# Kernel optimization log

Hardware: AMD Instinct MI355X
Metric: run time of the kernel (lower is better)

The kernel has to match this reference:

```python
import jax, jax.numpy as jnp
import numpy as np

NUM_EMB = 4096
EMB_DIM = 256
COMMIT = 0.25


def setup_inputs() -> dict:
    key = jax.random.key(0)
    k1, k2 = jax.random.split(key)
    z = jax.random.normal(k1, (64, 32, 32, EMB_DIM), dtype=jnp.float32)
    # torch init: uniform(-1/K, 1/K)
    codebook = jax.random.uniform(k2, (NUM_EMB, EMB_DIM), dtype=jnp.float32,
                                  minval=-1.0 / NUM_EMB, maxval=1.0 / NUM_EMB)
    return {"z": z, "codebook": codebook}


def reference(z, codebook):
    zf = z.reshape(-1, EMB_DIM)                       # [N, D]
    # ||z||^2 - 2 z.e + ||e||^2  -> [N, K]
    d = (jnp.sum(zf * zf, axis=1, keepdims=True)
         - 2.0 * (zf @ codebook.T)
         + jnp.sum(codebook * codebook, axis=1))
    idx = jnp.argmin(d, axis=1)                       # [N]
    z_q = codebook[idx].reshape(z.shape)              # gather replaces one-hot matmul
    sg = jax.lax.stop_gradient
    loss = jnp.mean((sg(z_q) - z) ** 2) + COMMIT * jnp.mean((z_q - sg(z)) ** 2)
    z_q_ste = z + sg(z_q - z)                         # straight-through
    return z_q_ste, loss
```

## Files before the change

kernel.cpp:

```cpp
#include <hip/hip_runtime.h>
#include <hip/hip_bf16.h>
#include <stdint.h>

#define NUM_EMB 4096
#define EMB_DIM 256
#define NVEC 65536
#define OUT0_SIZE (NVEC * EMB_DIM)
#define MTILE 128
#define NTILE 64
#define DCONST 0.0625f

typedef __bf16 bf16x8 __attribute__((ext_vector_type(8)));
typedef float floatx16 __attribute__((ext_vector_type(16)));

static __device__ __forceinline__ unsigned int f2bf(float f) {
  unsigned int u = __float_as_uint(f);
  return (u + 0x7fffu + ((u >> 16) & 1u)) >> 16;
}

static __device__ __forceinline__ uint4 pack_bf8(float4 a, float4 b) {
  uint4 r;
  r.x = f2bf(a.x) | (f2bf(a.y) << 16);
  r.y = f2bf(a.z) | (f2bf(a.w) << 16);
  r.z = f2bf(b.x) | (f2bf(b.y) << 16);
  r.w = f2bf(b.z) | (f2bf(b.w) << 16);
  return r;
}

__global__ void __launch_bounds__(256) vq_prep(const float* __restrict__ cbf,
                                               unsigned short* __restrict__ cbb,
                                               float* __restrict__ enorm,
                                               float* __restrict__ out) {
  int w = threadIdx.x >> 6;
  int lane = threadIdx.x & 63;
  int row = blockIdx.x * 4 + w;
  float4 v = ((const float4*)(cbf + (size_t)row * EMB_DIM))[lane];
  float ss = v.x * v.x + v.y * v.y + v.z * v.z + v.w * v.w;
  ushort4 b;
  b.x = (unsigned short)f2bf(v.x);
  b.y = (unsigned short)f2bf(v.y);
  b.z = (unsigned short)f2bf(v.z);
  b.w = (unsigned short)f2bf(v.w);
  ((ushort4*)(cbb + (size_t)row * EMB_DIM))[lane] = b;
#pragma unroll
  for (int m = 1; m < 64; m <<= 1) ss += __shfl_xor(ss, m, 64);
  if (lane == 0) enorm[row] = ss + DCONST;
  if (blockIdx.x == 0 && threadIdx.x == 0) out[OUT0_SIZE] = 0.0f;
}

__global__ void __launch_bounds__(256, 2) vq_main(const float* __restrict__ z,
                                                  const float* __restrict__ cbf,
                                                  const unsigned short* __restrict__ cbb,
                                                  const float* __restrict__ enorm,
                                                  float* __restrict__ out) {
  __shared__ __align__(16) unsigned char sstage[2][NTILE * 512];
  __shared__ unsigned int minlds[2][MTILE];
  __shared__ int idx_lds[MTILE];
  __shared__ float wsum[4];
  __shared__ float zwsum[2];

  const int t = threadIdx.x;
  const int w = t >> 6;
  const int lane = t & 63;
  const int h = lane >> 5;
  const int eL = lane & 31;
  const int rg = w & 1;
  const int cg = w >> 1;
  const int blk = blockIdx.x;
  const int row_base = blk * MTILE + rg * 64;

  auto stage_tile = [&](int buf, int c0) {
#pragma unroll
    for (int j = 0; j < 8; ++j) {
      int e = (w << 4) + (j << 1) + h;
      int s = eL ^ (e & 7);
      const unsigned short* src = cbb + ((size_t)(c0 + e) << 8) + (s << 3);
      __builtin_amdgcn_global_load_lds(
          (const __attribute__((address_space(1))) void*)src,
          (__attribute__((address_space(3))) void*)&sstage[buf][(w << 13) + (j << 10)],
          16, 0, 0);
    }
  };

  stage_tile(0, 0);
  float enC = enorm[cg * 32 + eL];

  uint4 afrag[2][16];
  float zn[2] = {0.f, 0.f};
#pragma unroll
  for (int g = 0; g < 2; ++g) {
    const float* rp = z + (size_t)(row_base + g * 32 + eL) * EMB_DIM + h * 8;
#pragma unroll
    for (int ks = 0; ks < 16; ++ks) {
      float4 a0 = *(const float4*)(rp + ks * 16);
      float4 a1 = *(const float4*)(rp + ks * 16 + 4);
      zn[g] += a0.x * a0.x + a0.y * a0.y + a0.z * a0.z + a0.w * a0.w
             + a1.x * a1.x + a1.y * a1.y + a1.z * a1.z + a1.w * a1.w;
      afrag[g][ks] = pack_bf8(a0, a1);
    }
    zn[g] += __shfl_xor(zn[g], 32, 64);
  }
  if (cg == 0) {
    float zs = zn[0] + zn[1];
#pragma unroll
    for (int m = 1; m <= 16; m <<= 1) zs += __shfl_xor(zs, m, 64);
    if (lane == 0) zwsum[rg] = zs;
  }

  unsigned int pmin[32];
#pragma unroll
  for (int s = 0; s < 32; ++s) pmin[s] = 0xFFFFFFFFu;

  __syncthreads();

  const int sx4 = (eL & 7) << 4;
  int cur = 0;
  for (int c0 = 0; c0 < NUM_EMB; c0 += NTILE) {
    int c1 = c0 + NTILE;
    float enN = enC;
    if (c1 < NUM_EMB) {
      stage_tile(cur ^ 1, c1);
      enN = enorm[c1 + cg * 32 + eL];
    }

    floatx16 acc0, acc1;
#pragma unroll
    for (int r = 0; r < 16; ++r) { acc0[r] = 0.f; acc1[r] = 0.f; }
    const unsigned char* bp = &sstage[cur][(cg * 32 + eL) * 512];
#pragma unroll
    for (int ks = 0; ks < 16; ++ks) {
      uint4 bv = *(const uint4*)(bp + ((ks * 32 + h * 16) ^ sx4));
      bf16x8 b = __builtin_bit_cast(bf16x8, bv);
      acc0 = __builtin_amdgcn_mfma_f32_32x32x16_bf16(
          __builtin_bit_cast(bf16x8, afrag[0][ks]), b, acc0, 0, 0, 0);
      acc1 = __builtin_amdgcn_mfma_f32_32x32x16_bf16(
          __builtin_bit_cast(bf16x8, afrag[1][ks]), b, acc1, 0, 0, 0);
    }

    unsigned int colb = (unsigned int)(c0 + cg * 32 + eL);
#pragma unroll
    for (int reg = 0; reg < 16; ++reg) {
      float d0 = fmaf(-2.f, acc0[reg], enC);
      unsigned int p0 = (__float_as_uint(d0) & 0xFFFFF000u) | colb;
      if (p0 < pmin[reg]) pmin[reg] = p0;
      float d1 = fmaf(-2.f, acc1[reg], enC);
      unsigned int p1 = (__float_as_uint(d1) & 0xFFFFF000u) | colb;
      if (p1 < pmin[16 + reg]) pmin[16 + reg] = p1;
    }

    __syncthreads();
    cur ^= 1;
    enC = enN;
  }

#pragma unroll
  for (int s = 0; s < 32; ++s) {
    unsigned int v = pmin[s];
#pragma unroll
    for (int m = 1; m <= 16; m <<= 1) {
      unsigned int o = __shfl_xor(v, m, 64);
      if (o < v) v = o;
    }
    pmin[s] = v;
  }
  if (eL == 0) {
#pragma unroll
    for (int s = 0; s < 32; ++s) {
      int g = s >> 4, reg = s & 15;
      int rowl = rg * 64 + g * 32 + (reg & 3) + 8 * (reg >> 2) + 4 * h;
      minlds[cg][rowl] = pmin[s];
    }
  }
  __syncthreads();

  float rl = 0.f;
  if (t < MTILE) {
    unsigned int m0 = minlds[0][t], m1 = minlds[1][t];
    unsigned int m = m1 < m0 ? m1 : m0;
    idx_lds[t] = (int)(m & 0xFFFu);
    rl = __uint_as_float(m & 0xFFFFF000u) - DCONST;
  }
#pragma unroll
  for (int m = 1; m < 64; m <<= 1) rl += __shfl_xor(rl, m, 64);
  if (lane == 0) wsum[w] = rl;
  __syncthreads();
  if (t == 0) {
    float s = (wsum[0] + wsum[1]) + (wsum[2] + wsum[3]) + zwsum[0] + zwsum[1];
    atomicAdd(out + OUT0_SIZE, s * (1.25f / (float)OUT0_SIZE));
  }

#pragma unroll 4
  for (int j = 0; j < 32; ++j) {
    int id4 = j * 256 + t;
    int r = id4 >> 6, c4 = id4 & 63;
    int k = idx_lds[r];
    float4 ev = ((const float4*)(cbf + (size_t)k * EMB_DIM))[c4];
    ((float4*)(out + (size_t)(blk * MTILE + r) * EMB_DIM))[c4] = ev;
  }
}

extern "C" void kernel_launch(void* const* d_in, const int* in_sizes, int n_in,
                              void* d_out, int out_size, void* d_ws, size_t ws_size,
                              hipStream_t stream) {
  const float* z = (const float*)d_in[0];
  const float* cbf = (const float*)d_in[1];
  unsigned short* cbb = (unsigned short*)d_ws;
  float* enorm = (float*)((char*)d_ws + (size_t)NUM_EMB * EMB_DIM * 2);
  float* out = (float*)d_out;
  vq_prep<<<NUM_EMB / 4, 256, 0, stream>>>(cbf, cbb, enorm, out);
  vq_main<<<NVEC / MTILE, 256, 0, stream>>>(z, cbf, cbb, enorm, out);
}
```

Measured before the change: 261.7 us.

## Software-pipeline argmin epilogue of previous tile under current tile's MFMAs

Unrolls the codebook loop by two with ping-pong accumulator sets, so the distance and argmin update for the previous 64-code tile interleaves with the MFMA chain of the current tile. The goal is to hide the VALU epilogue behind matrix-core latency rather than running it serially after each tile. The cost is an extra 32 accumulator registers per lane, which could raise VGPR/AGPR pressure under launch_bounds(256,2) and cause spills.

```diff
diff --git a/kernel.cpp b/kernel.cpp
--- a/kernel.cpp
+++ b/kernel.cpp
@@ -83,7 +83,7 @@
   };
 
   stage_tile(0, 0);
-  float enC = enorm[cg * 32 + eL];
+  const int laneoff = cg * 32 + eL;
 
   uint4 afrag[2][16];
   float zn[2] = {0.f, 0.f};
@@ -111,46 +111,68 @@
 #pragma unroll
   for (int s = 0; s < 32; ++s) pmin[s] = 0xFFFFFFFFu;
 
+  floatx16 fz;
+#pragma unroll
+  for (int r = 0; r < 16; ++r) fz[r] = 0.f;
+  floatx16 accE0, accE1, accO0, accO1;
+
   __syncthreads();
 
   const int sx4 = (eL & 7) << 4;
-  int cur = 0;
-  for (int c0 = 0; c0 < NUM_EMB; c0 += NTILE) {
-    int c1 = c0 + NTILE;
-    float enN = enC;
-    if (c1 < NUM_EMB) {
-      stage_tile(cur ^ 1, c1);
-      enN = enorm[c1 + cg * 32 + eL];
-    }
-
-    floatx16 acc0, acc1;
-#pragma unroll
-    for (int r = 0; r < 16; ++r) { acc0[r] = 0.f; acc1[r] = 0.f; }
-    const unsigned char* bp = &sstage[cur][(cg * 32 + eL) * 512];
+  const unsigned char* bpE = &sstage[0][(size_t)laneoff * 512];
+  const unsigned char* bpO = &sstage[1][(size_t)laneoff * 512];
+
+  auto half_step = [&](floatx16& a0, floatx16& a1, const floatx16& p0,
+                       const floatx16& p1, const unsigned char* bp,
+                       bool do_epi, unsigned int colbP, float enP) {
 #pragma unroll
     for (int ks = 0; ks < 16; ++ks) {
       uint4 bv = *(const uint4*)(bp + ((ks * 32 + h * 16) ^ sx4));
       bf16x8 b = __builtin_bit_cast(bf16x8, bv);
-      acc0 = __builtin_amdgcn_mfma_f32_32x32x16_bf16(
-          __builtin_bit_cast(bf16x8, afrag[0][ks]), b, acc0, 0, 0, 0);
-      acc1 = __builtin_amdgcn_mfma_f32_32x32x16_bf16(
-          __builtin_bit_cast(bf16x8, afrag[1][ks]), b, acc1, 0, 0, 0);
-    }
-
-    unsigned int colb = (unsigned int)(c0 + cg * 32 + eL);
-#pragma unroll
-    for (int reg = 0; reg < 16; ++reg) {
-      float d0 = fmaf(-2.f, acc0[reg], enC);
-      unsigned int p0 = (__float_as_uint(d0) & 0xFFFFF000u) | colb;
-      if (p0 < pmin[reg]) pmin[reg] = p0;
-      float d1 = fmaf(-2.f, acc1[reg], enC);
-      unsigned int p1 = (__float_as_uint(d1) & 0xFFFFF000u) | colb;
-      if (p1 < pmin[16 + reg]) pmin[16 + reg] = p1;
-    }
-
+      a0 = __builtin_amdgcn_mfma_f32_32x32x16_bf16(
+          __builtin_bit_cast(bf16x8, afrag[0][ks]), b, ks == 0 ? fz : a0, 0, 0, 0);
+      a1 = __builtin_amdgcn_mfma_f32_32x32x16_bf16(
+          __builtin_bit_cast(bf16x8, afrag[1][ks]), b, ks == 0 ? fz : a1, 0, 0, 0);
+      if (do_epi) {
+        float d0 = fmaf(-2.f, p0[ks], enP);
+        unsigned int q0 = (__float_as_uint(d0) & 0xFFFFF000u) | colbP;
+        pmin[ks] = min(pmin[ks], q0);
+        float d1 = fmaf(-2.f, p1[ks], enP);
+        unsigned int q1 = (__float_as_uint(d1) & 0xFFFFF000u) | colbP;
+        pmin[16 + ks] = min(pmin[16 + ks], q1);
+      }
+    }
+  };
+
+  float enE = enorm[laneoff];
+  float enOdd = 0.f;
+  for (int c0 = 0; c0 < NUM_EMB; c0 += 2 * NTILE) {
+    stage_tile(1, c0 + NTILE);
+    float enOn = enorm[c0 + NTILE + laneoff];
+    half_step(accE0, accE1, accO0, accO1, bpE, c0 > 0,
+              (unsigned int)(c0 - NTILE + laneoff), enOdd);
+    enOdd = enOn;
     __syncthreads();
-    cur ^= 1;
-    enC = enN;
+
+    float enEn = enE;
+    if (c0 + 2 * NTILE < NUM_EMB) {
+      stage_tile(0, c0 + 2 * NTILE);
+      enEn = enorm[c0 + 2 * NTILE + laneoff];
+    }
+    half_step(accO0, accO1, accE0, accE1, bpO, true,
+              (unsigned int)(c0 + laneoff), enE);
+    enE = enEn;
+    __syncthreads();
+  }
+#pragma unroll
+  for (int r = 0; r < 16; ++r) {
+    unsigned int colbP = (unsigned int)(NUM_EMB - NTILE + laneoff);
+    float d0 = fmaf(-2.f, accO0[r], enOdd);
+    unsigned int q0 = (__float_as_uint(d0) & 0xFFFFF000u) | colbP;
+    pmin[r] = min(pmin[r], q0);
+    float d1 = fmaf(-2.f, accO1[r], enOdd);
+    unsigned int q1 = (__float_as_uint(d1) & 0xFFFFF000u) | colbP;
+    pmin[16 + r] = min(pmin[16 + r], q1);
   }
 
 #pragma unroll
```

Result: slower. 370.4 us (+41.5%).

## Software-pipeline argmin epilogue into MFMA chains with interleaved scheduling

Applied to the files above, without the earlier changes.

The codebook loop is unrolled by two tiles, and the distance/argmin epilogue of each accumulator is overlapped with the MFMA chain of the other accumulator. Sched-group barriers interleave the MFMA, LDS read and VALU work, so the epilogue VALU cost is meant to hide under matrix-core latency. This raises live register pressure because both accumulators are held across chains, and it adds tricky bookkeeping for the enorm and column values of the previous tile.

```diff
diff --git a/kernel.cpp b/kernel.cpp
--- a/kernel.cpp
+++ b/kernel.cpp
@@ -48,6 +48,30 @@
   if (blockIdx.x == 0 && threadIdx.x == 0) out[OUT0_SIZE] = 0.0f;
 }
 
+#define ZERO16(ACC)                                   \
+  {                                                   \
+    _Pragma("unroll") for (int r_ = 0; r_ < 16; ++r_) \
+        (ACC)[r_] = 0.f;                              \
+  }
+
+#define CHAIN(BP, ACC, AG, PACC, POFF, DOEPI, ENP, COLBP)                     \
+  {                                                                           \
+    _Pragma("unroll") for (int ks_ = 0; ks_ < 16; ++ks_) {                    \
+      uint4 bv_ = *(const uint4*)((BP) + ((ks_ * 32 + h * 16) ^ sx4));        \
+      bf16x8 bb_ = __builtin_bit_cast(bf16x8, bv_);                           \
+      ACC = __builtin_amdgcn_mfma_f32_32x32x16_bf16(                          \
+          __builtin_bit_cast(bf16x8, afrag[AG][ks_]), bb_, ACC, 0, 0, 0);     \
+      if (DOEPI) {                                                            \
+        float d_ = fmaf(-2.f, (PACC)[ks_], (ENP));                            \
+        unsigned int q_ = (__float_as_uint(d_) & 0xFFFFF000u) | (COLBP);      \
+        pmin[(POFF) + ks_] = min(pmin[(POFF) + ks_], q_);                     \
+        __builtin_amdgcn_sched_group_barrier(0x100, 1, 0);                    \
+        __builtin_amdgcn_sched_group_barrier(0x008, 1, 0);                    \
+        __builtin_amdgcn_sched_group_barrier(0x002, 3, 0);                    \
+      }                                                                       \
+    }                                                                         \
+  }
+
 __global__ void __launch_bounds__(256, 2) vq_main(const float* __restrict__ z,
                                                   const float* __restrict__ cbf,
                                                   const unsigned short* __restrict__ cbb,
@@ -83,7 +107,7 @@
   };
 
   stage_tile(0, 0);
-  float enC = enorm[cg * 32 + eL];
+  const int laneoff = cg * 32 + eL;
 
   uint4 afrag[2][16];
   float zn[2] = {0.f, 0.f};
@@ -111,46 +135,58 @@
 #pragma unroll
   for (int s = 0; s < 32; ++s) pmin[s] = 0xFFFFFFFFu;
 
+  floatx16 acc0, acc1;
+
   __syncthreads();
 
   const int sx4 = (eL & 7) << 4;
-  int cur = 0;
-  for (int c0 = 0; c0 < NUM_EMB; c0 += NTILE) {
-    int c1 = c0 + NTILE;
-    float enN = enC;
-    if (c1 < NUM_EMB) {
-      stage_tile(cur ^ 1, c1);
-      enN = enorm[c1 + cg * 32 + eL];
-    }
-
-    floatx16 acc0, acc1;
-#pragma unroll
-    for (int r = 0; r < 16; ++r) { acc0[r] = 0.f; acc1[r] = 0.f; }
-    const unsigned char* bp = &sstage[cur][(cg * 32 + eL) * 512];
-#pragma unroll
-    for (int ks = 0; ks < 16; ++ks) {
-      uint4 bv = *(const uint4*)(bp + ((ks * 32 + h * 16) ^ sx4));
-      bf16x8 b = __builtin_bit_cast(bf16x8, bv);
-      acc0 = __builtin_amdgcn_mfma_f32_32x32x16_bf16(
-          __builtin_bit_cast(bf16x8, afrag[0][ks]), b, acc0, 0, 0, 0);
-      acc1 = __builtin_amdgcn_mfma_f32_32x32x16_bf16(
-          __builtin_bit_cast(bf16x8, afrag[1][ks]), b, acc1, 0, 0, 0);
-    }
-
-    unsigned int colb = (unsigned int)(c0 + cg * 32 + eL);
-#pragma unroll
-    for (int reg = 0; reg < 16; ++reg) {
-      float d0 = fmaf(-2.f, acc0[reg], enC);
-      unsigned int p0 = (__float_as_uint(d0) & 0xFFFFF000u) | colb;
-      if (p0 < pmin[reg]) pmin[reg] = p0;
-      float d1 = fmaf(-2.f, acc1[reg], enC);
-      unsigned int p1 = (__float_as_uint(d1) & 0xFFFFF000u) | colb;
-      if (p1 < pmin[16 + reg]) pmin[16 + reg] = p1;
-    }
-
+  const unsigned char* bpE = &sstage[0][(size_t)laneoff * 512];
+  const unsigned char* bpO = &sstage[1][(size_t)laneoff * 512];
+
+  float enC = enorm[laneoff];
+  float enP = 0.f;
+  unsigned int colbC = (unsigned int)laneoff;
+  unsigned int colbP = 0u;
+  float enN;
+
+  for (int c0 = 0; c0 < NUM_EMB; c0 += 2 * NTILE) {
+    stage_tile(1, c0 + NTILE);
+    enN = enorm[c0 + NTILE + laneoff];
+    ZERO16(acc0);
+    if (c0 == 0) {
+      CHAIN(bpE, acc0, 0, acc1, 16, 0, 0.f, 0u);
+    } else {
+      CHAIN(bpE, acc0, 0, acc1, 16, 1, enP, colbP);
+    }
+    asm volatile("" ::: "memory");
+    ZERO16(acc1);
+    CHAIN(bpE, acc1, 1, acc0, 0, 1, enC, colbC);
+    enP = enC; colbP = colbC;
+    enC = enN; colbC = (unsigned int)(c0 + NTILE + laneoff);
     __syncthreads();
-    cur ^= 1;
-    enC = enN;
+
+    int c2 = c0 + 2 * NTILE;
+    if (c2 < NUM_EMB) {
+      stage_tile(0, c2);
+      enN = enorm[c2 + laneoff];
+    }
+    ZERO16(acc0);
+    CHAIN(bpO, acc0, 0, acc1, 16, 1, enP, colbP);
+    asm volatile("" ::: "memory");
+    ZERO16(acc1);
+    CHAIN(bpO, acc1, 1, acc0, 0, 1, enC, colbC);
+    enP = enC; colbP = colbC;
+    if (c2 < NUM_EMB) {
+      enC = enN;
+      colbC = (unsigned int)(c2 + laneoff);
+    }
+    __syncthreads();
+  }
+#pragma unroll
+  for (int r = 0; r < 16; ++r) {
+    float d = fmaf(-2.f, acc1[r], enP);
+    unsigned int q = (__float_as_uint(d) & 0xFFFFF000u) | colbP;
+    pmin[16 + r] = min(pmin[16 + r], q);
   }
 
 #pragma unroll
```

New measurement: 418.7 us. 1.6x slower.

## Split 128-row tile across eight waves with one MFMA accumulator per wave

Applied to the files above, without the earlier changes.

Raises vq_main from 256 to 512 threads per block, giving each of eight waves a 32-row by 32-code sub-tile in place of 64x32. This halves per-wave A fragments, accumulators and running minima, cutting register pressure so more waves can be resident to hide LDS and global latency. Codebook staging, the final reductions and the gather loop are redistributed over the larger block. In exchange, each B fragment read from LDS now feeds one MFMA instead of two, doubling LDS read traffic per MFMA, and there are more waves per barrier.

```diff
diff --git a/kernel.cpp b/kernel.cpp
--- a/kernel.cpp
+++ b/kernel.cpp
@@ -48,7 +48,7 @@
   if (blockIdx.x == 0 && threadIdx.x == 0) out[OUT0_SIZE] = 0.0f;
 }
 
-__global__ void __launch_bounds__(256, 2) vq_main(const float* __restrict__ z,
+__global__ void __launch_bounds__(512, 4) vq_main(const float* __restrict__ z,
                                                   const float* __restrict__ cbf,
                                                   const unsigned short* __restrict__ cbb,
                                                   const float* __restrict__ enorm,
@@ -56,96 +56,91 @@
   __shared__ __align__(16) unsigned char sstage[2][NTILE * 512];
   __shared__ unsigned int minlds[2][MTILE];
   __shared__ int idx_lds[MTILE];
-  __shared__ float wsum[4];
-  __shared__ float zwsum[2];
+  __shared__ float wsum[8];
+  __shared__ float zwsum[4];
 
   const int t = threadIdx.x;
   const int w = t >> 6;
   const int lane = t & 63;
   const int h = lane >> 5;
   const int eL = lane & 31;
-  const int rg = w & 1;
-  const int cg = w >> 1;
+  const int rg = w >> 1;
+  const int cg = w & 1;
   const int blk = blockIdx.x;
-  const int row_base = blk * MTILE + rg * 64;
+  const int row_base = blk * MTILE + rg * 32;
 
   auto stage_tile = [&](int buf, int c0) {
 #pragma unroll
-    for (int j = 0; j < 8; ++j) {
-      int e = (w << 4) + (j << 1) + h;
+    for (int j = 0; j < 4; ++j) {
+      int e = (w << 3) + (j << 1) + h;
       int s = eL ^ (e & 7);
       const unsigned short* src = cbb + ((size_t)(c0 + e) << 8) + (s << 3);
       __builtin_amdgcn_global_load_lds(
           (const __attribute__((address_space(1))) void*)src,
-          (__attribute__((address_space(3))) void*)&sstage[buf][(w << 13) + (j << 10)],
+          (__attribute__((address_space(3))) void*)&sstage[buf][(w << 12) + (j << 10)],
           16, 0, 0);
     }
   };
 
   stage_tile(0, 0);
-  float enC = enorm[cg * 32 + eL];
-
-  uint4 afrag[2][16];
-  float zn[2] = {0.f, 0.f};
-#pragma unroll
-  for (int g = 0; g < 2; ++g) {
-    const float* rp = z + (size_t)(row_base + g * 32 + eL) * EMB_DIM + h * 8;
+  const int laneoff = cg * 32 + eL;
+
+  uint4 afrag[16];
+  float zn = 0.f;
+  {
+    const float* rp = z + (size_t)(row_base + eL) * EMB_DIM + h * 8;
 #pragma unroll
     for (int ks = 0; ks < 16; ++ks) {
       float4 a0 = *(const float4*)(rp + ks * 16);
       float4 a1 = *(const float4*)(rp + ks * 16 + 4);
-      zn[g] += a0.x * a0.x + a0.y * a0.y + a0.z * a0.z + a0.w * a0.w
-             + a1.x * a1.x + a1.y * a1.y + a1.z * a1.z + a1.w * a1.w;
-      afrag[g][ks] = pack_bf8(a0, a1);
-    }
-    zn[g] += __shfl_xor(zn[g], 32, 64);
+      zn += a0.x * a0.x + a0.y * a0.y + a0.z * a0.z + a0.w * a0.w
+          + a1.x * a1.x + a1.y * a1.y + a1.z * a1.z + a1.w * a1.w;
+      afrag[ks] = pack_bf8(a0, a1);
+    }
+    zn += __shfl_xor(zn, 32, 64);
   }
   if (cg == 0) {
-    float zs = zn[0] + zn[1];
+    float zs = zn;
 #pragma unroll
     for (int m = 1; m <= 16; m <<= 1) zs += __shfl_xor(zs, m, 64);
     if (lane == 0) zwsum[rg] = zs;
   }
 
-  unsigned int pmin[32];
-#pragma unroll
-  for (int s = 0; s < 32; ++s) pmin[s] = 0xFFFFFFFFu;
+  unsigned int pmin[16];
+#pragma unroll
+  for (int s = 0; s < 16; ++s) pmin[s] = 0xFFFFFFFFu;
 
   __syncthreads();
 
   const int sx4 = (eL & 7) << 4;
   int cur = 0;
+  float enC = enorm[laneoff];
   for (int c0 = 0; c0 < NUM_EMB; c0 += NTILE) {
     int c1 = c0 + NTILE;
     float enN = enC;
     if (c1 < NUM_EMB) {
       stage_tile(cur ^ 1, c1);
-      enN = enorm[c1 + cg * 32 + eL];
-    }
-
-    floatx16 acc0, acc1;
-#pragma unroll
-    for (int r = 0; r < 16; ++r) { acc0[r] = 0.f; acc1[r] = 0.f; }
-    const unsigned char* bp = &sstage[cur][(cg * 32 + eL) * 512];
+      enN = enorm[c1 + laneoff];
+    }
+
+    floatx16 acc;
+#pragma unroll
+    for (int r = 0; r < 16; ++r) acc[r] = 0.f;
+    const unsigned char* bp = &sstage[cur][(size_t)laneoff * 512];
 #pragma unroll
     for (int ks = 0; ks < 16; ++ks) {
       uint4 bv = *(const uint4*)(bp + ((ks * 32 + h * 16) ^ sx4));
       bf16x8 b = __builtin_bit_cast(bf16x8, bv);
-      acc0 = __builtin_amdgcn_mfma_f32_32x32x16_bf16(
-          __builtin_bit_cast(bf16x8, afrag[0][ks]), b, acc0, 0, 0, 0);
-      acc1 = __builtin_amdgcn_mfma_f32_32x32x16_bf16(
-          __builtin_bit_cast(bf16x8, afrag[1][ks]), b, acc1, 0, 0, 0);
-    }
-
-    unsigned int colb = (unsigned int)(c0 + cg * 32 + eL);
+      acc = __builtin_amdgcn_mfma_f32_32x32x16_bf16(
+          __builtin_bit_cast(bf16x8, afrag[ks]), b, acc, 0, 0, 0);
+    }
+
+    unsigned int colb = (unsigned int)(c0 + laneoff);
 #pragma unroll
     for (int reg = 0; reg < 16; ++reg) {
-      float d0 = fmaf(-2.f, acc0[reg], enC);
-      unsigned int p0 = (__float_as_uint(d0) & 0xFFFFF000u) | colb;
-      if (p0 < pmin[reg]) pmin[reg] = p0;
-      float d1 = fmaf(-2.f, acc1[reg], enC);
-      unsigned int p1 = (__float_as_uint(d1) & 0xFFFFF000u) | colb;
-      if (p1 < pmin[16 + reg]) pmin[16 + reg] = p1;
+      float d = fmaf(-2.f, acc[reg], enC);
+      unsigned int p = (__float_as_uint(d) & 0xFFFFF000u) | colb;
+      pmin[reg] = min(pmin[reg], p);
     }
 
     __syncthreads();
@@ -154,7 +149,7 @@
   }
 
 #pragma unroll
-  for (int s = 0; s < 32; ++s) {
+  for (int s = 0; s < 16; ++s) {
     unsigned int v = pmin[s];
 #pragma unroll
     for (int m = 1; m <= 16; m <<= 1) {
@@ -165,9 +160,8 @@
   }
   if (eL == 0) {
 #pragma unroll
-    for (int s = 0; s < 32; ++s) {
-      int g = s >> 4, reg = s & 15;
-      int rowl = rg * 64 + g * 32 + (reg & 3) + 8 * (reg >> 2) + 4 * h;
+    for (int s = 0; s < 16; ++s) {
+      int rowl = rg * 32 + (s & 3) + 8 * (s >> 2) + 4 * h;
       minlds[cg][rowl] = pmin[s];
     }
   }
@@ -185,13 +179,15 @@
   if (lane == 0) wsum[w] = rl;
   __syncthreads();
   if (t == 0) {
-    float s = (wsum[0] + wsum[1]) + (wsum[2] + wsum[3]) + zwsum[0] + zwsum[1];
+    float s = ((wsum[0] + wsum[1]) + (wsum[2] + wsum[3]))
+            + ((wsum[4] + wsum[5]) + (wsum[6] + wsum[7]))
+            + (zwsum[0] + zwsum[1]) + (zwsum[2] + zwsum[3]);
     atomicAdd(out + OUT0_SIZE, s * (1.25f / (float)OUT0_SIZE));
   }
 
 #pragma unroll 4
-  for (int j = 0; j < 32; ++j) {
-    int id4 = j * 256 + t;
+  for (int j = 0; j < 16; ++j) {
+    int id4 = j * 512 + t;
     int r = id4 >> 6, c4 = id4 & 63;
     int k = idx_lds[r];
     float4 ev = ((const float4*)(cbf + (size_t)k * EMB_DIM))[c4];
@@ -208,5 +204,5 @@
   float* enorm = (float*)((char*)d_ws + (size_t)NUM_EMB * EMB_DIM * 2);
   float* out = (float*)d_out;
   vq_prep<<<NUM_EMB / 4, 256, 0, stream>>>(cbf, cbb, enorm, out);
-  vq_main<<<NVEC / MTILE, 256, 0, stream>>>(z, cbf, cbb, enorm, out);
-}
+  vq_main<<<NVEC / MTILE, 512, 0, stream>>>(z, cbf, cbb, enorm, out);
+}
```

Result: slower. 299.4 us (+14.4%).
